# Kernel tuning notes

Measured on AMD Instinct MI355X. Metric: run time of the kernel, lower is better.

Reference implementation:

```python
import jax, jax.numpy as jnp
import numpy as np

B, S, D, H, F = 16, 512, 1024, 16, 4096
DH = D // H
LN_EPS = 1e-12


def layer_norm(x, g, b):
    mu = jnp.mean(x, axis=-1, keepdims=True)
    var = jnp.mean(jnp.square(x - mu), axis=-1, keepdims=True)
    return (x - mu) * jax.lax.rsqrt(var + LN_EPS) * g + b


def setup_inputs() -> dict:
    key = jax.random.key(0)
    ks = jax.random.split(key, 16)
    s_attn = 1.0 / np.sqrt(D)
    s_ffn = 1.0 / np.sqrt(F)
    return {
        "hidden_states": jax.random.normal(ks[0], (B, S, D), jnp.float32),
        "attention_mask": jnp.zeros((B, S), jnp.float32),
        # weights stored [in, out]
        "Wq": jax.random.normal(ks[1], (D, D), jnp.float32) * s_attn,
        "bq": jnp.zeros((D,), jnp.float32),
        "Wk": jax.random.normal(ks[2], (D, D), jnp.float32) * s_attn,
        "bk": jnp.zeros((D,), jnp.float32),
        "Wv": jax.random.normal(ks[3], (D, D), jnp.float32) * s_attn,
        "bv": jnp.zeros((D,), jnp.float32),
        "Wo": jax.random.normal(ks[4], (D, D), jnp.float32) * s_attn,
        "bo": jnp.zeros((D,), jnp.float32),
        "ln1_g": jnp.ones((D,), jnp.float32),
        "ln1_b": jnp.zeros((D,), jnp.float32),
        "Wi": jax.random.normal(ks[5], (D, F), jnp.float32) * s_attn,
        "bi": jnp.zeros((F,), jnp.float32),
        "Wo2": jax.random.normal(ks[6], (F, D), jnp.float32) * s_ffn,
        "bo2": jnp.zeros((D,), jnp.float32),
        "ln2_g": jnp.ones((D,), jnp.float32),
        "ln2_b": jnp.zeros((D,), jnp.float32),
    }


def reference(hidden_states, attention_mask, Wq, bq, Wk, bk, Wv, bv, Wo, bo,
              ln1_g, ln1_b, Wi, bi, Wo2, bo2, ln2_g, ln2_b):
    x = hidden_states
    # --- self attention ---
    q = (x @ Wq + bq).reshape(B, S, H, DH)
    k = (x @ Wk + bk).reshape(B, S, H, DH)
    v = (x @ Wv + bv).reshape(B, S, H, DH)
    scores = jnp.einsum("bqhd,bkhd->bhqk", q, k) / np.sqrt(DH)
    scores = scores + attention_mask[:, None, None, :]
    probs = jax.nn.softmax(scores, axis=-1)  # dropout p=0 (eval)
    ctx = jnp.einsum("bhqk,bkhd->bqhd", probs, v).reshape(B, S, D)
    # --- self output: dense + residual + LN ---
    attn_out = layer_norm(ctx @ Wo + bo + x, ln1_g, ln1_b)
    # --- intermediate: dense + gelu (exact erf gelu, BERT) ---
    inter = jax.nn.gelu(attn_out @ Wi + bi, approximate=False)
    # --- output: dense + residual + LN ---
    out = layer_norm(inter @ Wo2 + bo2 + attn_out, ln2_g, ln2_b)
    return out
```

## Files before the change

### kernel.cpp

```cpp
#include <hip/hip_runtime.h>
#include <hip/hip_bf16.h>
#include <math.h>

#define DEV_INLINE __device__ __forceinline__

typedef __attribute__((ext_vector_type(8))) short bf16x8;
typedef __attribute__((ext_vector_type(8))) unsigned short u16x8;
typedef __attribute__((ext_vector_type(4))) float f32x4;


DEV_INLINE void gload_lds16(const void* g, void* l) {
  __builtin_amdgcn_global_load_lds(
      (__attribute__((address_space(1))) unsigned int*)const_cast<void*>(g),
      (__attribute__((address_space(3))) unsigned int*)l,
      16, 0, 0);
}

DEV_INLINE unsigned lds_a(const void* p) {
  return (unsigned)(unsigned long long)(__attribute__((address_space(3))) const void*)p;
}

DEV_INLINE short f2bs(float x) {
  union { __hip_bfloat16 h; short s; } u;
  u.h = __float2bfloat16(x);
  return u.s;
}

DEV_INLINE f32x4 mfma16(bf16x8 a, bf16x8 b, f32x4 c) {
  return __builtin_amdgcn_mfma_f32_16x16x32_bf16(a, b, c, 0, 0, 0);
}

#define DSREAD_O(dst, base, imm) \
  asm volatile("ds_read_b128 %0, %1 offset:%2" : "=v"(dst) : "v"(base), "n"(imm))


__global__ __launch_bounds__(256)
void cvt_x_bf16(const float* __restrict__ in, __hip_bfloat16* __restrict__ out) {
  const size_t i = ((size_t)blockIdx.x * 256 + threadIdx.x) * 4;
  const float4 x = *(const float4*)(in + i);
  union { __hip_bfloat16 h[4]; ushort4 u; } pk;
  pk.h[0] = __float2bfloat16(x.x);
  pk.h[1] = __float2bfloat16(x.y);
  pk.h[2] = __float2bfloat16(x.z);
  pk.h[3] = __float2bfloat16(x.w);
  *(ushort4*)(out + i) = pk.u;
}

__global__ __launch_bounds__(256)
void transpose_w(const float* __restrict__ W, __hip_bfloat16* __restrict__ Wt, int K, int N) {
  __shared__ float t[32][33];
  const int n0 = blockIdx.x * 32, k0 = blockIdx.y * 32;
  const int tx = threadIdx.x & 31, ty = threadIdx.x >> 5;
#pragma unroll
  for (int r = ty; r < 32; r += 8)
    t[r][tx] = W[(size_t)(k0 + r) * N + n0 + tx];
  __syncthreads();
#pragma unroll
  for (int r = ty; r < 32; r += 8)
    Wt[(size_t)(n0 + r) * K + k0 + tx] = __float2bfloat16(t[tx][r]);
}

__global__ __launch_bounds__(256)
void concat_bias(const float* __restrict__ a, const float* __restrict__ b,
                 const float* __restrict__ c, float* __restrict__ o) {
  const int i = blockIdx.x * 256 + threadIdx.x;
  o[i] = a[i]; o[1024 + i] = b[i]; o[2048 + i] = c[i];
}


template<int MODE>
DEV_INLINE void gemm256_body(const short* __restrict__ A, const short* __restrict__ Bt,
                             const float* __restrict__ bias,
                             __hip_bfloat16* __restrict__ Cb,
                             int M, int N, int K)
{
  __shared__ __align__(128) short lds[24576];

  const int tid = threadIdx.x;
  const int lane = tid & 63, wid = tid >> 6;
  const int q4 = lane >> 4, c16 = lane & 15;
  const int wm = (wid >> 1) * 64, wn = (wid & 1) * 64;

  const int nNT = N >> 7;
  int bid = blockIdx.x;
  { const int cpx = (int)gridDim.x >> 3; bid = (bid & 7) * cpx + (bid >> 3); }
  const int bm = (bid / nNT) * 256;
  const int bn = (bid % nNT) * 128;

  const int sr = tid >> 3, sl = tid & 7;
  const int sg = (sl ^ (sr & 7)) * 8;
  const short* pA = A  + (size_t)(bm + sr) * K + sg;
  const short* pB = Bt + (size_t)(bn + sr) * K + sg;
  char* const baseA = (char*)lds;
  char* const baseB = (char*)lds + 32768;

  f32x4 acc[4][4];
#pragma unroll
  for (int i = 0; i < 4; ++i)
#pragma unroll
    for (int j = 0; j < 4; ++j) acc[i][j] = (f32x4){0.f, 0.f, 0.f, 0.f};

  for (int kt = 0; kt < K; kt += 64) {
    __syncthreads();
#pragma unroll
    for (int u = 0; u < 4; ++u)
      gload_lds16(pA + (size_t)u * 64 * K + kt, baseA + u * 8192 + wid * 1024);
#pragma unroll
    for (int u = 0; u < 2; ++u)
      gload_lds16(pB + (size_t)u * 64 * K + kt, baseB + u * 8192 + wid * 1024);
    __syncthreads();

#pragma unroll
    for (int kk = 0; kk < 2; ++kk) {
      bf16x8 af[4], bfr[4];
#pragma unroll
      for (int mt = 0; mt < 4; ++mt)
        af[mt] = *(const bf16x8*)(baseA + (wm + mt * 16 + c16) * 128 +
                                  (((kk * 4 + q4) ^ (c16 & 7)) * 16));
#pragma unroll
      for (int nt = 0; nt < 4; ++nt)
        bfr[nt] = *(const bf16x8*)(baseB + (wn + nt * 16 + c16) * 128 +
                                   (((kk * 4 + q4) ^ (c16 & 7)) * 16));
#pragma unroll
      for (int mt = 0; mt < 4; ++mt)
#pragma unroll
        for (int nt = 0; nt < 4; ++nt)
          acc[mt][nt] = mfma16(af[mt], bfr[nt], acc[mt][nt]);
    }
  }

  __syncthreads();

  float* eb = (float*)((char*)lds + wid * 4352);
  const int erow = lane >> 2, ecol = (lane & 3) * 16;
#pragma unroll
  for (int mf = 0; mf < 4; ++mf) {
#pragma unroll
    for (int nf = 0; nf < 4; ++nf) {
      const int col = bn + wn + nf * 16 + c16;
      const float bsv = bias[col];
#pragma unroll
      for (int j = 0; j < 4; ++j) {
        float v = acc[mf][nf][j] + bsv;
        if constexpr (MODE == 2)
          v = 0.5f * v * (1.0f + erff(v * 0.70710678118654752f));
        eb[(q4 * 4 + j) * 68 + nf * 16 + c16] = v;
      }
    }
    const int gr = bm + wm + mf * 16 + erow;
    const size_t gbase = (size_t)gr * N + bn + wn + ecol;
    unsigned short* cp = (unsigned short*)Cb;
#pragma unroll
    for (int u = 0; u < 2; ++u) {
      float4 a = *(float4*)&eb[erow * 68 + ecol + u * 8];
      float4 b = *(float4*)&eb[erow * 68 + ecol + u * 8 + 4];
      u16x8 o;
      o[0] = (unsigned short)f2bs(a.x); o[1] = (unsigned short)f2bs(a.y);
      o[2] = (unsigned short)f2bs(a.z); o[3] = (unsigned short)f2bs(a.w);
      o[4] = (unsigned short)f2bs(b.x); o[5] = (unsigned short)f2bs(b.y);
      o[6] = (unsigned short)f2bs(b.z); o[7] = (unsigned short)f2bs(b.w);
      *(u16x8*)(cp + gbase + u * 8) = o;
    }
  }
}


template<int MODE>
DEV_INLINE void gemm64_body(const short* __restrict__ A, const short* __restrict__ Bt,
                            const float* __restrict__ bias, const float* __restrict__ resid,
                            __hip_bfloat16* __restrict__ Cb, float* __restrict__ Cf,
                            int M, int N, int K)
{
  __shared__ __align__(128) short lds[32768];

  const int tid = threadIdx.x;
  const int lane = tid & 63, w = tid >> 6;
  const int q4 = lane >> 4, c16 = lane & 15;
  const int wm = (w >> 1) * 64, wn = (w & 1) * 64;

  const int nNT = N >> 7;
  int bid = blockIdx.x;
  { const int cpx = (int)gridDim.x >> 3; bid = (bid & 7) * cpx + (bid >> 3); }
  const int bm = (bid / nNT) * 128;
  const int bn = (bid % nNT) * 128;

  const int sr = tid >> 3, sl = tid & 7;
  const int sg = (sl ^ (sr & 7)) * 8;
  const short* pA = A  + (size_t)(bm + sr) * K + sg;
  const short* pB = Bt + (size_t)(bn + sr) * K + sg;

  const int s0 = (q4 ^ (c16 & 7)) * 16;
  const int s1 = ((q4 ^ 4) ^ (c16 & 7)) * 16;
  unsigned aRd0 = lds_a(lds) + (unsigned)((wm + c16) * 128 + s0);
  unsigned aRd1 = lds_a(lds) + (unsigned)((wm + c16) * 128 + s1);
  unsigned bRd0 = lds_a(lds) + (unsigned)(16384 + (wn + c16) * 128 + s0);
  unsigned bRd1 = lds_a(lds) + (unsigned)(16384 + (wn + c16) * 128 + s1);

  f32x4 acc[4][4];
#pragma unroll
  for (int i = 0; i < 4; ++i)
#pragma unroll
    for (int j = 0; j < 4; ++j) acc[i][j] = (f32x4){0.f, 0.f, 0.f, 0.f};

  auto stage = [&](int buf, int kt) {
    char* b = (char*)lds + buf * 32768;
#pragma unroll
    for (int u = 0; u < 4; ++u) {
      gload_lds16(pA + (size_t)u * 32 * K + kt, b + u * 4096 + w * 1024);
      gload_lds16(pB + (size_t)u * 32 * K + kt, b + 16384 + u * 4096 + w * 1024);
    }
  };

  stage(0, 0);
  __syncthreads();

  const int NT = K >> 6;
  int cur = 0;
  for (int t = 0; t < NT; ++t) {
    __builtin_amdgcn_sched_barrier(0);
    if (t + 1 < NT) stage(cur ^ 1, (t + 1) << 6);
    __builtin_amdgcn_sched_barrier(0);

    bf16x8 a0, a1, a2, a3, a4, a5, a6, a7;
    bf16x8 b0, b1, b2, b3, b4, b5, b6, b7;
    DSREAD_O(a0, aRd0, 0 * 2048); DSREAD_O(a1, aRd0, 1 * 2048);
    DSREAD_O(a2, aRd0, 2 * 2048); DSREAD_O(a3, aRd0, 3 * 2048);
    DSREAD_O(b0, bRd0, 0 * 2048); DSREAD_O(b1, bRd0, 1 * 2048);
    DSREAD_O(b2, bRd0, 2 * 2048); DSREAD_O(b3, bRd0, 3 * 2048);
    DSREAD_O(a4, aRd1, 0 * 2048); DSREAD_O(a5, aRd1, 1 * 2048);
    DSREAD_O(a6, aRd1, 2 * 2048); DSREAD_O(a7, aRd1, 3 * 2048);
    DSREAD_O(b4, bRd1, 0 * 2048); DSREAD_O(b5, bRd1, 1 * 2048);
    DSREAD_O(b6, bRd1, 2 * 2048); DSREAD_O(b7, bRd1, 3 * 2048);

    asm volatile("s_waitcnt lgkmcnt(0)");
    __builtin_amdgcn_sched_barrier(0);
    __builtin_amdgcn_s_setprio(1);
    acc[0][0] = mfma16(a0, b0, acc[0][0]); acc[0][1] = mfma16(a0, b1, acc[0][1]);
    acc[0][2] = mfma16(a0, b2, acc[0][2]); acc[0][3] = mfma16(a0, b3, acc[0][3]);
    acc[1][0] = mfma16(a1, b0, acc[1][0]); acc[1][1] = mfma16(a1, b1, acc[1][1]);
    acc[1][2] = mfma16(a1, b2, acc[1][2]); acc[1][3] = mfma16(a1, b3, acc[1][3]);
    acc[2][0] = mfma16(a2, b0, acc[2][0]); acc[2][1] = mfma16(a2, b1, acc[2][1]);
    acc[2][2] = mfma16(a2, b2, acc[2][2]); acc[2][3] = mfma16(a2, b3, acc[2][3]);
    acc[3][0] = mfma16(a3, b0, acc[3][0]); acc[3][1] = mfma16(a3, b1, acc[3][1]);
    acc[3][2] = mfma16(a3, b2, acc[3][2]); acc[3][3] = mfma16(a3, b3, acc[3][3]);
    acc[0][0] = mfma16(a4, b4, acc[0][0]); acc[0][1] = mfma16(a4, b5, acc[0][1]);
    acc[0][2] = mfma16(a4, b6, acc[0][2]); acc[0][3] = mfma16(a4, b7, acc[0][3]);
    acc[1][0] = mfma16(a5, b4, acc[1][0]); acc[1][1] = mfma16(a5, b5, acc[1][1]);
    acc[1][2] = mfma16(a5, b6, acc[1][2]); acc[1][3] = mfma16(a5, b7, acc[1][3]);
    acc[2][0] = mfma16(a6, b4, acc[2][0]); acc[2][1] = mfma16(a6, b5, acc[2][1]);
    acc[2][2] = mfma16(a6, b6, acc[2][2]); acc[2][3] = mfma16(a6, b7, acc[2][3]);
    acc[3][0] = mfma16(a7, b4, acc[3][0]); acc[3][1] = mfma16(a7, b5, acc[3][1]);
    acc[3][2] = mfma16(a7, b6, acc[3][2]); acc[3][3] = mfma16(a7, b7, acc[3][3]);
    __builtin_amdgcn_s_setprio(0);

    __syncthreads();
    aRd0 ^= 0x8000; aRd1 ^= 0x8000; bRd0 ^= 0x8000; bRd1 ^= 0x8000; cur ^= 1;
  }

  float* eb = (float*)((char*)lds + w * 4352);
  const int erow = lane >> 2, ecol = (lane & 3) * 16;
#pragma unroll
  for (int mf = 0; mf < 4; ++mf) {
#pragma unroll
    for (int nf = 0; nf < 4; ++nf) {
      const int col = bn + wn + nf * 16 + c16;
      const float bsv = bias[col];
#pragma unroll
      for (int j = 0; j < 4; ++j) {
        float v = acc[mf][nf][j] + bsv;
        if constexpr (MODE == 2)
          v = 0.5f * v * (1.0f + erff(v * 0.70710678118654752f));
        eb[(q4 * 4 + j) * 68 + nf * 16 + c16] = v;
      }
    }
    const int gr = bm + wm + mf * 16 + erow;
    const size_t gbase = (size_t)gr * N + bn + wn + ecol;
    if constexpr (MODE == 1) {
#pragma unroll
      for (int u = 0; u < 4; ++u) {
        float4 t = *(float4*)&eb[erow * 68 + ecol + u * 4];
        const float4 r = *(const float4*)&resid[gbase + u * 4];
        t.x += r.x; t.y += r.y; t.z += r.z; t.w += r.w;
        *(float4*)&Cf[gbase + u * 4] = t;
      }
    } else {
      unsigned short* cp = (unsigned short*)Cb;
#pragma unroll
      for (int u = 0; u < 2; ++u) {
        float4 a = *(float4*)&eb[erow * 68 + ecol + u * 8];
        float4 b = *(float4*)&eb[erow * 68 + ecol + u * 8 + 4];
        u16x8 o;
        o[0] = (unsigned short)f2bs(a.x); o[1] = (unsigned short)f2bs(a.y);
        o[2] = (unsigned short)f2bs(a.z); o[3] = (unsigned short)f2bs(a.w);
        o[4] = (unsigned short)f2bs(b.x); o[5] = (unsigned short)f2bs(b.y);
        o[6] = (unsigned short)f2bs(b.z); o[7] = (unsigned short)f2bs(b.w);
        *(u16x8*)(cp + gbase + u * 8) = o;
      }
    }
  }
}

__global__ __launch_bounds__(512)
void gemm_qkv(const short* A, const short* Bt, const float* bias,
              __hip_bfloat16* Cb, int M, int N, int K) {
  gemm256_body<0>(A, Bt, bias, Cb, M, N, K);
}
__global__ __launch_bounds__(512)
void gemm_wi(const short* A, const short* Bt, const float* bias,
             __hip_bfloat16* Cb, int M, int N, int K) {
  gemm256_body<2>(A, Bt, bias, Cb, M, N, K);
}
__global__ __launch_bounds__(256)
void gemm_wo(const short* A, const short* Bt, const float* bias,
             const float* resid, float* Cf, int M, int N, int K) {
  gemm64_body<1>(A, Bt, bias, resid, nullptr, Cf, M, N, K);
}
__global__ __launch_bounds__(256)
void gemm_wo2(const short* A, const short* Bt, const float* bias,
              const float* resid, float* Cf, int M, int N, int K) {
  gemm64_body<1>(A, Bt, bias, resid, nullptr, Cf, M, N, K);
}


__global__ __launch_bounds__(256)
void attn_flash(const short* __restrict__ Q, const short* __restrict__ Kmat,
                const short* __restrict__ V, const float* __restrict__ mask,
                __hip_bfloat16* __restrict__ ctx, int qs)
{
  __shared__ short Ksm[64 * 64];
  __shared__ short Vsm[64 * 64];
  __shared__ short Psm[4 * 16 * 64];

  const int tid = threadIdx.x;
  const int lane = tid & 63;
  const int w = tid >> 6;
  const int q4 = lane >> 4;
  const int c16 = lane & 15;
  const int b = blockIdx.z;
  const int h = blockIdx.y;
  const int qb = blockIdx.x;

  const size_t rowbase = (size_t)b * 512;
  const int hoff = h * 64;

  bf16x8 aq[2];
  {
    const size_t qrow = rowbase + (size_t)qb * 64 + w * 16 + c16;
    const short* qp = Q + qrow * qs + hoff + q4 * 8;
    aq[0] = *(const bf16x8*)(qp);
    aq[1] = *(const bf16x8*)(qp + 32);
  }

  float m_r[4], l_r[4];
  f32x4 O[4];
#pragma unroll
  for (int j = 0; j < 4; ++j) { m_r[j] = -INFINITY; l_r[j] = 0.f; O[j] = (f32x4){0.f, 0.f, 0.f, 0.f}; }

  const int kc0 = w * 128 + lane;
  const int kp0 = kc0 >> 3, kd0 = (kc0 & 7) * 8;
  const int kc1 = kc0 + 64;
  const int kp1 = kc1 >> 3, kd1 = (kc1 & 7) * 8;

  for (int kv0 = 0; kv0 < 512; kv0 += 64) {
    __syncthreads();
    gload_lds16(Kmat + (rowbase + kv0 + kp0) * qs + hoff + (kd0 ^ ((kp0 & 7) << 3)),
                (char*)Ksm + (size_t)(w * 128 + 0) * 16);
    gload_lds16(Kmat + (rowbase + kv0 + kp1) * qs + hoff + (kd1 ^ ((kp1 & 7) << 3)),
                (char*)Ksm + (size_t)(w * 128 + 64) * 16);
#pragma unroll
    for (int it = 0; it < 2; ++it) {
      const int c = tid + 256 * it;
      const int kp = c >> 3;
      const int dh8 = (c & 7) * 8;
      const bf16x8 vv = *(const bf16x8*)(V + (rowbase + kv0 + kp) * qs + hoff + dh8);
#pragma unroll
      for (int j = 0; j < 8; ++j) {
        const int dh = dh8 + j;
        *(short*)((char*)Vsm + dh * 128 + ((kp * 2) ^ ((dh & 7) << 4))) = vv[j];
      }
    }
    __syncthreads();

    float pv[4][4];
    float mk[4];
#pragma unroll
    for (int t = 0; t < 4; ++t) mk[t] = mask[rowbase + kv0 + t * 16 + c16];
#pragma unroll
    for (int t = 0; t < 4; ++t) {
      f32x4 z = (f32x4){0.f, 0.f, 0.f, 0.f};
      const int kp = t * 16 + c16;
#pragma unroll
      for (int ks = 0; ks < 2; ++ks) {
        const int d = ks * 32 + q4 * 8;
        bf16x8 kf = *(const bf16x8*)((char*)Ksm + kp * 128 + ((d * 2) ^ ((kp & 7) << 4)));
        z = mfma16(aq[ks], kf, z);
      }
#pragma unroll
      for (int j = 0; j < 4; ++j) pv[t][j] = z[j] * 0.125f + mk[t];
    }

#pragma unroll
    for (int j = 0; j < 4; ++j) {
      float mt_ = fmaxf(fmaxf(pv[0][j], pv[1][j]), fmaxf(pv[2][j], pv[3][j]));
#pragma unroll
      for (int o = 8; o >= 1; o >>= 1) mt_ = fmaxf(mt_, __shfl_xor(mt_, o));
      const float mn = fmaxf(m_r[j], mt_);
      const float sc = __expf(m_r[j] - mn);
      float rs = 0.f;
#pragma unroll
      for (int t = 0; t < 4; ++t) { const float pe = __expf(pv[t][j] - mn); pv[t][j] = pe; rs += pe; }
#pragma unroll
      for (int o = 8; o >= 1; o >>= 1) rs += __shfl_xor(rs, o);
      l_r[j] = l_r[j] * sc + rs;
      m_r[j] = mn;
#pragma unroll
      for (int nt = 0; nt < 4; ++nt) O[nt][j] *= sc;
    }

    char* pb = (char*)Psm + w * 2048;
#pragma unroll
    for (int j = 0; j < 4; ++j) {
      const int r = q4 * 4 + j;
#pragma unroll
      for (int t = 0; t < 4; ++t) {
        const int ck = t * 16 + c16;
        *(short*)(pb + r * 128 + ((ck * 2) ^ ((r & 7) << 4))) = f2bs(pv[t][j]);
      }
    }

#pragma unroll
    for (int ks = 0; ks < 2; ++ks) {
      const int kk = ks * 32 + q4 * 8;
      bf16x8 pa = *(const bf16x8*)(pb + c16 * 128 + ((kk * 2) ^ ((c16 & 7) << 4)));
#pragma unroll
      for (int nt = 0; nt < 4; ++nt) {
        const int dh = nt * 16 + c16;
        bf16x8 vf = *(const bf16x8*)((char*)Vsm + dh * 128 + ((kk * 2) ^ ((dh & 7) << 4)));
        O[nt] = mfma16(pa, vf, O[nt]);
      }
    }
  }

  float rinv[4];
#pragma unroll
  for (int j = 0; j < 4; ++j) rinv[j] = 1.0f / l_r[j];
#pragma unroll
  for (int nt = 0; nt < 4; ++nt) {
#pragma unroll
    for (int j = 0; j < 4; ++j) {
      const size_t row = rowbase + (size_t)qb * 64 + w * 16 + q4 * 4 + j;
      ctx[row * 1024 + hoff + nt * 16 + c16] = __float2bfloat16(O[nt][j] * rinv[j]);
    }
  }
}


DEV_INLINE void ln_body(const float* __restrict__ in, const float* __restrict__ gam,
                        const float* __restrict__ bet, float* __restrict__ outf,
                        __hip_bfloat16* __restrict__ outb)
{
  const int row = blockIdx.x;
  const int tid = threadIdx.x;
  const size_t base = (size_t)row * 1024 + tid * 4;
  const float4 x = *(const float4*)(in + base);
  float s  = x.x + x.y + x.z + x.w;
  float s2 = x.x * x.x + x.y * x.y + x.z * x.z + x.w * x.w;
#pragma unroll
  for (int o = 32; o >= 1; o >>= 1) { s += __shfl_xor(s, o); s2 += __shfl_xor(s2, o); }
  __shared__ float sb[8];
  const int w = tid >> 6;
  if ((tid & 63) == 0) { sb[w] = s; sb[w + 4] = s2; }
  __syncthreads();
  const float ts  = sb[0] + sb[1] + sb[2] + sb[3];
  const float ts2 = sb[4] + sb[5] + sb[6] + sb[7];
  const float mu = ts * (1.0f / 1024.0f);
  const float var = ts2 * (1.0f / 1024.0f) - mu * mu;
  const float rstd = rsqrtf(var + 1e-12f);
  const float4 g4 = *(const float4*)(gam + tid * 4);
  const float4 b4 = *(const float4*)(bet + tid * 4);
  const float y0 = (x.x - mu) * rstd * g4.x + b4.x;
  const float y1 = (x.y - mu) * rstd * g4.y + b4.y;
  const float y2 = (x.z - mu) * rstd * g4.z + b4.z;
  const float y3 = (x.w - mu) * rstd * g4.w + b4.w;
  if (outf) {
    float4 y; y.x = y0; y.y = y1; y.z = y2; y.w = y3;
    *(float4*)(outf + base) = y;
  }
  if (outb) {
    union { __hip_bfloat16 h[4]; ushort4 u; } pk;
    pk.h[0] = __float2bfloat16(y0);
    pk.h[1] = __float2bfloat16(y1);
    pk.h[2] = __float2bfloat16(y2);
    pk.h[3] = __float2bfloat16(y3);
    *(ushort4*)(outb + base) = pk.u;
  }
}

__global__ __launch_bounds__(256)
void ln_attn(const float* in, const float* gam, const float* bet,
             float* outf, __hip_bfloat16* outb) { ln_body(in, gam, bet, outf, outb); }
__global__ __launch_bounds__(256)
void ln_ffn(const float* in, const float* gam, const float* bet, float* outf) {
  ln_body(in, gam, bet, outf, nullptr);
}


extern "C" void kernel_launch(void* const* d_in, const int* in_sizes, int n_in,
                              void* d_out, int out_size, void* d_ws, size_t ws_size,
                              hipStream_t stream)
{
  const float* X    = (const float*)d_in[0];
  const float* mask = (const float*)d_in[1];
  const float* Wq   = (const float*)d_in[2];   const float* bq  = (const float*)d_in[3];
  const float* Wk   = (const float*)d_in[4];   const float* bk  = (const float*)d_in[5];
  const float* Wv   = (const float*)d_in[6];   const float* bv  = (const float*)d_in[7];
  const float* Wo   = (const float*)d_in[8];   const float* bo  = (const float*)d_in[9];
  const float* g1   = (const float*)d_in[10];  const float* b1  = (const float*)d_in[11];
  const float* Wi   = (const float*)d_in[12];  const float* bi  = (const float*)d_in[13];
  const float* Wo2  = (const float*)d_in[14];  const float* bo2 = (const float*)d_in[15];
  const float* g2   = (const float*)d_in[16];  const float* b2  = (const float*)d_in[17];
  float* out = (float*)d_out;
  (void)in_sizes; (void)n_in; (void)out_size; (void)ws_size;

  const size_t D = 1024, F = 4096;
  const size_t MN = 8192 * D;

  char* p = (char*)d_ws;
  auto alloc = [&](size_t bytes) { char* r = p; p += (bytes + 255) & ~(size_t)255; return r; };
  short* Xb    = (short*)alloc(MN * 2);
  short* QKVb  = (short*)alloc(8192 * 3072 * 2);
  short* WqkvT = (short*)alloc(3072 * D * 2);
  short* WoT   = (short*)alloc(D * D * 2);
  short* WiT   = (short*)alloc(D * F * 2);
  short* Wo2T  = (short*)alloc(D * F * 2);
  float* bqkv  = (float*)alloc(3072 * 4);
  float* A1f   = (float*)alloc(MN * 4);
  short* I1    = (short*)alloc(8192 * F * 2);

  cvt_x_bf16<<<dim3((unsigned)(MN / 1024)), 256, 0, stream>>>(X, (__hip_bfloat16*)Xb);
  transpose_w<<<dim3(32, 32),  256, 0, stream>>>(Wq,  (__hip_bfloat16*)(WqkvT + 0),           1024, 1024);
  transpose_w<<<dim3(32, 32),  256, 0, stream>>>(Wk,  (__hip_bfloat16*)(WqkvT + 1024 * 1024), 1024, 1024);
  transpose_w<<<dim3(32, 32),  256, 0, stream>>>(Wv,  (__hip_bfloat16*)(WqkvT + 2048 * 1024), 1024, 1024);
  transpose_w<<<dim3(32, 32),  256, 0, stream>>>(Wo,  (__hip_bfloat16*)WoT,  1024, 1024);
  transpose_w<<<dim3(128, 32), 256, 0, stream>>>(Wi,  (__hip_bfloat16*)WiT,  1024, 4096);
  transpose_w<<<dim3(32, 128), 256, 0, stream>>>(Wo2, (__hip_bfloat16*)Wo2T, 4096, 1024);
  concat_bias<<<dim3(4), 256, 0, stream>>>(bq, bk, bv, bqkv);

  gemm_qkv<<<dim3(768), 512, 0, stream>>>(Xb, WqkvT, bqkv, (__hip_bfloat16*)QKVb, 8192, 3072, 1024);

  attn_flash<<<dim3(8, 16, 16), 256, 0, stream>>>(QKVb, QKVb + 1024, QKVb + 2048, mask,
                                                  (__hip_bfloat16*)Xb, 3072);

  gemm_wo<<<dim3(512), 256, 0, stream>>>(Xb, WoT, bo, X, out, 8192, 1024, 1024);
  ln_attn<<<dim3(8192), 256, 0, stream>>>(out, g1, b1, A1f, (__hip_bfloat16*)QKVb);

  gemm_wi<<<dim3(1024), 512, 0, stream>>>(QKVb, WiT, bi, (__hip_bfloat16*)I1, 8192, 4096, 1024);

  gemm_wo2<<<dim3(512), 256, 0, stream>>>(I1, Wo2T, bo2, A1f, out, 8192, 1024, 4096);
  ln_ffn<<<dim3(8192), 256, 0, stream>>>(out, g2, b2, out);
}
```

Before: 395.3 us.

## Store residual-stream intermediates in bf16 and merge prep kernels into one launch

```diff
diff --git a/kernel.cpp b/kernel.cpp
--- a/kernel.cpp
+++ b/kernel.cpp
@@ -26,6 +26,12 @@
   return u.s;
 }
 
+DEV_INLINE float bs2f(unsigned short s) {
+  union { float f; unsigned u; } v;
+  v.u = ((unsigned)s) << 16;
+  return v.f;
+}
+
 DEV_INLINE f32x4 mfma16(bf16x8 a, bf16x8 b, f32x4 c) {
   return __builtin_amdgcn_mfma_f32_16x16x32_bf16(a, b, c, 0, 0, 0);
 }
@@ -35,36 +41,55 @@
 
 
 __global__ __launch_bounds__(256)
-void cvt_x_bf16(const float* __restrict__ in, __hip_bfloat16* __restrict__ out) {
-  const size_t i = ((size_t)blockIdx.x * 256 + threadIdx.x) * 4;
-  const float4 x = *(const float4*)(in + i);
-  union { __hip_bfloat16 h[4]; ushort4 u; } pk;
-  pk.h[0] = __float2bfloat16(x.x);
-  pk.h[1] = __float2bfloat16(x.y);
-  pk.h[2] = __float2bfloat16(x.z);
-  pk.h[3] = __float2bfloat16(x.w);
-  *(ushort4*)(out + i) = pk.u;
-}
-
-__global__ __launch_bounds__(256)
-void transpose_w(const float* __restrict__ W, __hip_bfloat16* __restrict__ Wt, int K, int N) {
+void prep_all(const float* __restrict__ X, __hip_bfloat16* __restrict__ Xb,
+              const float* __restrict__ Wq, const float* __restrict__ Wk,
+              const float* __restrict__ Wv, const float* __restrict__ Wo,
+              const float* __restrict__ Wi, const float* __restrict__ Wo2,
+              __hip_bfloat16* __restrict__ WqkvT, __hip_bfloat16* __restrict__ WoT,
+              __hip_bfloat16* __restrict__ WiT, __hip_bfloat16* __restrict__ Wo2T,
+              const float* __restrict__ bq, const float* __restrict__ bk,
+              const float* __restrict__ bv, float* __restrict__ bqkv)
+{
+  int bx = blockIdx.x;
+  const int tid = threadIdx.x;
+
+  if (bx < 8192) {
+    const size_t i = ((size_t)bx * 256 + tid) * 4;
+    const float4 x = *(const float4*)(X + i);
+    union { __hip_bfloat16 h[4]; ushort4 u; } pk;
+    pk.h[0] = __float2bfloat16(x.x);
+    pk.h[1] = __float2bfloat16(x.y);
+    pk.h[2] = __float2bfloat16(x.z);
+    pk.h[3] = __float2bfloat16(x.w);
+    *(ushort4*)(Xb + i) = pk.u;
+    return;
+  }
+  bx -= 8192;
+  if (bx < 4) {
+    const int i = bx * 256 + tid;
+    bqkv[i] = bq[i]; bqkv[1024 + i] = bk[i]; bqkv[2048 + i] = bv[i];
+    return;
+  }
+  bx -= 4;
+
+  const float* Wsrc; __hip_bfloat16* Wdst; int K, N, nt, kt;
+  if (bx < 1024)      { Wsrc = Wq;  Wdst = WqkvT;               K = 1024; N = 1024; nt = bx & 31;  kt = bx >> 5; }
+  else if (bx < 2048) { const int l = bx - 1024; Wsrc = Wk;  Wdst = WqkvT + 1024 * 1024; K = 1024; N = 1024; nt = l & 31;  kt = l >> 5; }
+  else if (bx < 3072) { const int l = bx - 2048; Wsrc = Wv;  Wdst = WqkvT + 2048 * 1024; K = 1024; N = 1024; nt = l & 31;  kt = l >> 5; }
+  else if (bx < 4096) { const int l = bx - 3072; Wsrc = Wo;  Wdst = WoT;  K = 1024; N = 1024; nt = l & 31;  kt = l >> 5; }
+  else if (bx < 8192) { const int l = bx - 4096; Wsrc = Wi;  Wdst = WiT;  K = 1024; N = 4096; nt = l & 127; kt = l >> 7; }
+  else                { const int l = bx - 8192; Wsrc = Wo2; Wdst = Wo2T; K = 4096; N = 1024; nt = l & 31;  kt = l >> 5; }
+
   __shared__ float t[32][33];
-  const int n0 = blockIdx.x * 32, k0 = blockIdx.y * 32;
-  const int tx = threadIdx.x & 31, ty = threadIdx.x >> 5;
+  const int n0 = nt * 32, k0 = kt * 32;
+  const int tx = tid & 31, ty = tid >> 5;
 #pragma unroll
   for (int r = ty; r < 32; r += 8)
-    t[r][tx] = W[(size_t)(k0 + r) * N + n0 + tx];
+    t[r][tx] = Wsrc[(size_t)(k0 + r) * N + n0 + tx];
   __syncthreads();
 #pragma unroll
   for (int r = ty; r < 32; r += 8)
-    Wt[(size_t)(n0 + r) * K + k0 + tx] = __float2bfloat16(t[tx][r]);
-}
-
-__global__ __launch_bounds__(256)
-void concat_bias(const float* __restrict__ a, const float* __restrict__ b,
-                 const float* __restrict__ c, float* __restrict__ o) {
-  const int i = blockIdx.x * 256 + threadIdx.x;
-  o[i] = a[i]; o[1024 + i] = b[i]; o[2048 + i] = c[i];
+    Wdst[(size_t)(n0 + r) * K + k0 + tx] = __float2bfloat16(t[tx][r]);
 }
 
 
@@ -167,8 +192,10 @@
 
 template<int MODE>
 DEV_INLINE void gemm64_body(const short* __restrict__ A, const short* __restrict__ Bt,
-                            const float* __restrict__ bias, const float* __restrict__ resid,
-                            __hip_bfloat16* __restrict__ Cb, float* __restrict__ Cf,
+                            const float* __restrict__ bias,
+                            const float* __restrict__ residf,
+                            const unsigned short* __restrict__ residb,
+                            __hip_bfloat16* __restrict__ Cb,
                             int M, int N, int K)
 {
   __shared__ __align__(128) short lds[32768];
@@ -266,36 +293,32 @@
       const int col = bn + wn + nf * 16 + c16;
       const float bsv = bias[col];
 #pragma unroll
-      for (int j = 0; j < 4; ++j) {
-        float v = acc[mf][nf][j] + bsv;
-        if constexpr (MODE == 2)
-          v = 0.5f * v * (1.0f + erff(v * 0.70710678118654752f));
-        eb[(q4 * 4 + j) * 68 + nf * 16 + c16] = v;
-      }
+      for (int j = 0; j < 4; ++j)
+        eb[(q4 * 4 + j) * 68 + nf * 16 + c16] = acc[mf][nf][j] + bsv;
     }
     const int gr = bm + wm + mf * 16 + erow;
     const size_t gbase = (size_t)gr * N + bn + wn + ecol;
-    if constexpr (MODE == 1) {
-#pragma unroll
-      for (int u = 0; u < 4; ++u) {
-        float4 t = *(float4*)&eb[erow * 68 + ecol + u * 4];
-        const float4 r = *(const float4*)&resid[gbase + u * 4];
-        t.x += r.x; t.y += r.y; t.z += r.z; t.w += r.w;
-        *(float4*)&Cf[gbase + u * 4] = t;
+    unsigned short* cp = (unsigned short*)Cb;
+#pragma unroll
+    for (int u = 0; u < 2; ++u) {
+      float4 a = *(float4*)&eb[erow * 68 + ecol + u * 8];
+      float4 b = *(float4*)&eb[erow * 68 + ecol + u * 8 + 4];
+      if constexpr (MODE == 3) {
+        const float4 ra = *(const float4*)&residf[gbase + u * 8];
+        const float4 rb = *(const float4*)&residf[gbase + u * 8 + 4];
+        a.x += ra.x; a.y += ra.y; a.z += ra.z; a.w += ra.w;
+        b.x += rb.x; b.y += rb.y; b.z += rb.z; b.w += rb.w;
+      } else {
+        const u16x8 rv = *(const u16x8*)(residb + gbase + u * 8);
+        a.x += bs2f(rv[0]); a.y += bs2f(rv[1]); a.z += bs2f(rv[2]); a.w += bs2f(rv[3]);
+        b.x += bs2f(rv[4]); b.y += bs2f(rv[5]); b.z += bs2f(rv[6]); b.w += bs2f(rv[7]);
       }
-    } else {
-      unsigned short* cp = (unsigned short*)Cb;
-#pragma unroll
-      for (int u = 0; u < 2; ++u) {
-        float4 a = *(float4*)&eb[erow * 68 + ecol + u * 8];
-        float4 b = *(float4*)&eb[erow * 68 + ecol + u * 8 + 4];
-        u16x8 o;
-        o[0] = (unsigned short)f2bs(a.x); o[1] = (unsigned short)f2bs(a.y);
-        o[2] = (unsigned short)f2bs(a.z); o[3] = (unsigned short)f2bs(a.w);
-        o[4] = (unsigned short)f2bs(b.x); o[5] = (unsigned short)f2bs(b.y);
-        o[6] = (unsigned short)f2bs(b.z); o[7] = (unsigned short)f2bs(b.w);
-        *(u16x8*)(cp + gbase + u * 8) = o;
-      }
+      u16x8 o;
+      o[0] = (unsigned short)f2bs(a.x); o[1] = (unsigned short)f2bs(a.y);
+      o[2] = (unsigned short)f2bs(a.z); o[3] = (unsigned short)f2bs(a.w);
+      o[4] = (unsigned short)f2bs(b.x); o[5] = (unsigned short)f2bs(b.y);
+      o[6] = (unsigned short)f2bs(b.z); o[7] = (unsigned short)f2bs(b.w);
+      *(u16x8*)(cp + gbase + u * 8) = o;
     }
   }
 }
@@ -312,13 +335,13 @@
 }
 __global__ __launch_bounds__(256)
 void gemm_wo(const short* A, const short* Bt, const float* bias,
-             const float* resid, float* Cf, int M, int N, int K) {
-  gemm64_body<1>(A, Bt, bias, resid, nullptr, Cf, M, N, K);
+             const float* residf, __hip_bfloat16* Cb, int M, int N, int K) {
+  gemm64_body<3>(A, Bt, bias, residf, nullptr, Cb, M, N, K);
 }
 __global__ __launch_bounds__(256)
 void gemm_wo2(const short* A, const short* Bt, const float* bias,
-              const float* resid, float* Cf, int M, int N, int K) {
-  gemm64_body<1>(A, Bt, bias, resid, nullptr, Cf, M, N, K);
+              const unsigned short* residb, __hip_bfloat16* Cb, int M, int N, int K) {
+  gemm64_body<4>(A, Bt, bias, nullptr, residb, Cb, M, N, K);
 }
 
 
@@ -455,16 +478,18 @@
 }
 
 
-DEV_INLINE void ln_body(const float* __restrict__ in, const float* __restrict__ gam,
+template<int OUTB>
+DEV_INLINE void ln_body(const unsigned short* __restrict__ in, const float* __restrict__ gam,
                         const float* __restrict__ bet, float* __restrict__ outf,
-                        __hip_bfloat16* __restrict__ outb)
+                        unsigned short* __restrict__ outb)
 {
   const int row = blockIdx.x;
   const int tid = threadIdx.x;
   const size_t base = (size_t)row * 1024 + tid * 4;
-  const float4 x = *(const float4*)(in + base);
-  float s  = x.x + x.y + x.z + x.w;
-  float s2 = x.x * x.x + x.y * x.y + x.z * x.z + x.w * x.w;
+  const ushort4 xi = *(const ushort4*)(in + base);
+  const float x0 = bs2f(xi.x), x1 = bs2f(xi.y), x2 = bs2f(xi.z), x3 = bs2f(xi.w);
+  float s  = x0 + x1 + x2 + x3;
+  float s2 = x0 * x0 + x1 * x1 + x2 * x2 + x3 * x3;
 #pragma unroll
   for (int o = 32; o >= 1; o >>= 1) { s += __shfl_xor(s, o); s2 += __shfl_xor(s2, o); }
   __shared__ float sb[8];
@@ -478,30 +503,27 @@
   const float rstd = rsqrtf(var + 1e-12f);
   const float4 g4 = *(const float4*)(gam + tid * 4);
   const float4 b4 = *(const float4*)(bet + tid * 4);
-  const float y0 = (x.x - mu) * rstd * g4.x + b4.x;
-  const float y1 = (x.y - mu) * rstd * g4.y + b4.y;
-  const float y2 = (x.z - mu) * rstd * g4.z + b4.z;
-  const float y3 = (x.w - mu) * rstd * g4.w + b4.w;
-  if (outf) {
+  const float y0 = (x0 - mu) * rstd * g4.x + b4.x;
+  const float y1 = (x1 - mu) * rstd * g4.y + b4.y;
+  const float y2 = (x2 - mu) * rstd * g4.z + b4.z;
+  const float y3 = (x3 - mu) * rstd * g4.w + b4.w;
+  if constexpr (OUTB) {
+    ushort4 o;
+    o.x = (unsigned short)f2bs(y0); o.y = (unsigned short)f2bs(y1);
+    o.z = (unsigned short)f2bs(y2); o.w = (unsigned short)f2bs(y3);
+    *(ushort4*)(outb + base) = o;
+  } else {
     float4 y; y.x = y0; y.y = y1; y.z = y2; y.w = y3;
     *(float4*)(outf + base) = y;
   }
-  if (outb) {
-    union { __hip_bfloat16 h[4]; ushort4 u; } pk;
-    pk.h[0] = __float2bfloat16(y0);
-    pk.h[1] = __float2bfloat16(y1);
-    pk.h[2] = __float2bfloat16(y2);
-    pk.h[3] = __float2bfloat16(y3);
-    *(ushort4*)(outb + base) = pk.u;
-  }
 }
 
 __global__ __launch_bounds__(256)
-void ln_attn(const float* in, const float* gam, const float* bet,
-             float* outf, __hip_bfloat16* outb) { ln_body(in, gam, bet, outf, outb); }
+void ln_attn(const unsigned short* in, const float* gam, const float* bet,
+             unsigned short* outb) { ln_body<1>(in, gam, bet, nullptr, outb); }
 __global__ __launch_bounds__(256)
-void ln_ffn(const float* in, const float* gam, const float* bet, float* outf) {
-  ln_body(in, gam, bet, outf, nullptr);
+void ln_ffn(const unsigned short* in, const float* gam, const float* bet, float* outf) {
+  ln_body<0>(in, gam, bet, outf, nullptr);
 }
 
 
@@ -534,28 +556,25 @@
   short* WiT   = (short*)alloc(D * F * 2);
   short* Wo2T  = (short*)alloc(D * F * 2);
   float* bqkv  = (float*)alloc(3072 * 4);
-  float* A1f   = (float*)alloc(MN * 4);
   short* I1    = (short*)alloc(8192 * F * 2);
 
-  cvt_x_bf16<<<dim3((unsigned)(MN / 1024)), 256, 0, stream>>>(X, (__hip_bfloat16*)Xb);
-  transpose_w<<<dim3(32, 32),  256, 0, stream>>>(Wq,  (__hip_bfloat16*)(WqkvT + 0),           1024, 1024);
-  transpose_w<<<dim3(32, 32),  256, 0, stream>>>(Wk,  (__hip_bfloat16*)(WqkvT + 1024 * 1024), 1024, 1024);
-  transpose_w<<<dim3(32, 32),  256, 0, stream>>>(Wv,  (__hip_bfloat16*)(WqkvT + 2048 * 1024), 1024, 1024);
-  transpose_w<<<dim3(32, 32),  256, 0, stream>>>(Wo,  (__hip_bfloat16*)WoT,  1024, 1024);
-  transpose_w<<<dim3(128, 32), 256, 0, stream>>>(Wi,  (__hip_bfloat16*)WiT,  1024, 4096);
-  transpose_w<<<dim3(32, 128), 256, 0, stream>>>(Wo2, (__hip_bfloat16*)Wo2T, 4096, 1024);
-  concat_bias<<<dim3(4), 256, 0, stream>>>(bq, bk, bv, bqkv);
+  prep_all<<<dim3(20484), 256, 0, stream>>>(X, (__hip_bfloat16*)Xb,
+                                            Wq, Wk, Wv, Wo, Wi, Wo2,
+                                            (__hip_bfloat16*)WqkvT, (__hip_bfloat16*)WoT,
+                                            (__hip_bfloat16*)WiT, (__hip_bfloat16*)Wo2T,
+                                            bq, bk, bv, bqkv);
 
   gemm_qkv<<<dim3(768), 512, 0, stream>>>(Xb, WqkvT, bqkv, (__hip_bfloat16*)QKVb, 8192, 3072, 1024);
 
   attn_flash<<<dim3(8, 16, 16), 256, 0, stream>>>(QKVb, QKVb + 1024, QKVb + 2048, mask,
                                                   (__hip_bfloat16*)Xb, 3072);
 
-  gemm_wo<<<dim3(512), 256, 0, stream>>>(Xb, WoT, bo, X, out, 8192, 1024, 1024);
-  ln_attn<<<dim3(8192), 256, 0, stream>>>(out, g1, b1, A1f, (__hip_bfloat16*)QKVb);
+  gemm_wo<<<dim3(512), 256, 0, stream>>>(Xb, WoT, bo, X, (__hip_bfloat16*)out, 8192, 1024, 1024);
+  ln_attn<<<dim3(8192), 256, 0, stream>>>((const unsigned short*)out, g1, b1, (unsigned short*)QKVb);
 
   gemm_wi<<<dim3(1024), 512, 0, stream>>>(QKVb, WiT, bi, (__hip_bfloat16*)I1, 8192, 4096, 1024);
 
-  gemm_wo2<<<dim3(512), 256, 0, stream>>>(I1, Wo2T, bo2, A1f, out, 8192, 1024, 4096);
-  ln_ffn<<<dim3(8192), 256, 0, stream>>>(out, g2, b2, out);
-}
+  gemm_wo2<<<dim3(512), 256, 0, stream>>>(I1, Wo2T, bo2, (const unsigned short*)QKVb,
+                                          (__hip_bfloat16*)Xb, 8192, 1024, 4096);
+  ln_ffn<<<dim3(8192), 256, 0, stream>>>((const unsigned short*)Xb, g2, b2, out);
+}
```

After: 359.2 us. 1.1x faster.
